# Optimization experiments

Hardware: AMD Instinct MI355X
Metric: run time of the kernel (lower is better)

The kernel has to match this reference:

```python
import jax, jax.numpy as jnp
import numpy as np


def setup_inputs() -> dict:
    key = jax.random.key(0)
    k1, k2, k3, k4 = jax.random.split(key, 4)
    B, N, F, T, K, O = 16, 1024, 16, 12, 3, 16
    x = jax.random.normal(k1, (B, N, F, T), dtype=jnp.float32)
    spatial_attention = jax.random.uniform(k2, (B, N, N), dtype=jnp.float32)
    adj = jax.random.uniform(k3, (N, N), dtype=jnp.float32)
    # xavier_uniform_ on [K, F, O]: bound = sqrt(6/(F+O)) over last two dims
    bound = float(np.sqrt(6.0 / (F + O)))
    Theta = jax.random.uniform(k4, (K, F, O), dtype=jnp.float32, minval=-bound, maxval=bound)
    return {"x": x, "spatial_attention": spatial_attention, "adj": adj, "Theta": Theta}


def reference(x, spatial_attention, adj, Theta):
    # x: [B, N, F, T], spatial_attention: [B, N, N], adj: [N, N], Theta: [K, F, O]
    B, N, F, T = x.shape
    K = Theta.shape[0]
    a = adj[None, :, :] * spatial_attention                      # [B, N, N]
    eye = jnp.broadcast_to(jnp.eye(N, dtype=x.dtype), (B, N, N))
    supports = [eye, a]
    for _ in range(2, K):                                        # power series of adjacency
        supports.append(jnp.matmul(supports[-1], a))
    S = jnp.stack(supports, axis=0)                              # [K, B, N, N]
    # rhs[k,b,n,f,t] = sum_m S[k,b,m,n] * x[b,m,f,t]  (supports[k]^T @ x), fused over T and K
    rhs = jnp.einsum('kbmn,bmft->kbnft', S, x)                   # [K, B, N, F, T]
    out = jnp.einsum('kbnft,kfo->bnot', rhs, Theta)              # [B, N, O, T]
    return jax.nn.relu(out)
```

## Files before the change

### kernel.cpp

```cpp
#include <hip/hip_runtime.h>
#include <hip/hip_bf16.h>


typedef __attribute__((ext_vector_type(8))) __bf16 bf16x8;
typedef __attribute__((ext_vector_type(4))) float  f32x4;
typedef __attribute__((ext_vector_type(8))) short  short8;
typedef __attribute__((ext_vector_type(4))) short  s16x4;

__device__ inline unsigned short f32_to_bf16(float f) {
    unsigned int u = __builtin_bit_cast(unsigned int, f);
    unsigned int r = u + 0x7FFFu + ((u >> 16) & 1u);
    return (unsigned short)(r >> 16);
}
__device__ inline float bf16_to_f32(unsigned short u) {
    unsigned int x = ((unsigned int)u) << 16;
    return __builtin_bit_cast(float, x);
}

__device__ inline void gload_lds16(const void* gsrc, void* ldst) {
    __builtin_amdgcn_global_load_lds(
        (const __attribute__((address_space(1))) unsigned int*)gsrc,
        (__attribute__((address_space(3))) unsigned int*)ldst,
        16, 0, 0);
}

__global__ void prep_a(const float* __restrict__ sa, const float* __restrict__ adj,
                       unsigned short* __restrict__ aT)
{
    __shared__ float tile[32][33];
    const int b  = blockIdx.z;
    const int m0 = blockIdx.y * 32;
    const int n0 = blockIdx.x * 32;
    const int tid = threadIdx.x;
    const int r  = tid >> 3;
    const int c4 = (tid & 7) * 4;
    const float* sab = sa + (size_t)b * 1024 * 1024;

    size_t idx = (size_t)(m0 + r) * 1024 + (n0 + c4);
    f32x4 av = *reinterpret_cast<const f32x4*>(&adj[idx]);
    f32x4 sv = *reinterpret_cast<const f32x4*>(&sab[idx]);
#pragma unroll
    for (int k = 0; k < 4; k++) tile[r][c4 + k] = av[k] * sv[k];
    __syncthreads();

    unsigned short* aTb = aT + (size_t)b * 1024 * 1024;
    const int nl = tid >> 3;
    const int m4 = (tid & 7) * 4;
    s16x4 v;
#pragma unroll
    for (int k = 0; k < 4; k++) v[k] = (short)f32_to_bf16(tile[m4 + k][nl]);
    *reinterpret_cast<s16x4*>(&aTb[(size_t)(n0 + nl) * 1024 + m0 + m4]) = v;
}

__global__ void prep_x(const float* __restrict__ x, unsigned short* __restrict__ xT)
{
    __shared__ float tile[32][33];
    const int b  = blockIdx.z;
    const int j0 = blockIdx.y * 32;
    const int m0 = blockIdx.x * 32;
    const int tid = threadIdx.x;
    const int r  = tid >> 3;
    const int c4 = (tid & 7) * 4;
    const float* xb = x + (size_t)b * 1024 * 192;

    f32x4 v = *reinterpret_cast<const f32x4*>(&xb[(size_t)(m0 + r) * 192 + j0 + c4]);
#pragma unroll
    for (int k = 0; k < 4; k++) tile[r][c4 + k] = v[k];
    __syncthreads();

    unsigned short* xTb = xT + (size_t)b * 192 * 1024;
    const int jl = tid >> 3;
    const int m4 = (tid & 7) * 4;
    s16x4 o;
#pragma unroll
    for (int k = 0; k < 4; k++) o[k] = (short)f32_to_bf16(tile[m4 + k][jl]);
    *reinterpret_cast<s16x4*>(&xTb[(size_t)(j0 + jl) * 1024 + m0 + m4]) = o;
}

__global__ __launch_bounds__(256, 2)
void gemm_tn(const unsigned short* __restrict__ Aop,
             const unsigned short* __restrict__ Bop,
             unsigned short* __restrict__ Cout)
{
    const int b  = blockIdx.z;
    const int j0 = blockIdx.y * 96;
    const int n0 = blockIdx.x * 64;
    const unsigned short* Ab = Aop + (size_t)b * 192 * 1024;
    const unsigned short* Bb = Bop + (size_t)b * 1024 * 1024;

    __shared__ unsigned short Blds[3][64 * 64];

    const int tid  = threadIdx.x;
    const int lane = tid & 63;
    const int wave = tid >> 6;
    const int wj   = wave >> 1;
    const int wn   = wave & 1;
    const int lr   = lane & 15;
    const int lg   = lane >> 4;

    const int srow = lane >> 3;
    const int sg16 = (lane & 7) ^ srow;

    f32x4 acc[3][2];
#pragma unroll
    for (int i = 0; i < 3; i++)
#pragma unroll
        for (int j = 0; j < 2; j++) acc[i][j] = f32x4{0.f, 0.f, 0.f, 0.f};

    const unsigned short* Arow[3];
#pragma unroll
    for (int ri = 0; ri < 3; ri++)
        Arow[ri] = Ab + (size_t)(j0 + wj * 48 + ri * 16 + lr) * 1024 + lg * 8;

    bf16x8 Ac[2][3], An[2][3];

#pragma unroll
    for (int i = 0; i < 2; i++) {
        int c = wave + i * 4;
        gload_lds16(Bb + (size_t)(n0 + 8 * c + srow) * 1024 + 0 + sg16 * 8,
                    &Blds[0][c * 512]);
    }
#pragma unroll
    for (int i = 0; i < 2; i++) {
        int c = wave + i * 4;
        gload_lds16(Bb + (size_t)(n0 + 8 * c + srow) * 1024 + 64 + sg16 * 8,
                    &Blds[1][c * 512]);
    }
#pragma unroll
    for (int h = 0; h < 2; h++)
#pragma unroll
        for (int ri = 0; ri < 3; ri++)
            Ac[h][ri] = __builtin_bit_cast(bf16x8,
                *reinterpret_cast<const short8*>(Arow[ri] + h * 32));
    __builtin_amdgcn_sched_barrier(0);
    asm volatile("s_waitcnt vmcnt(8)" ::: "memory");
    __builtin_amdgcn_s_barrier();
    __builtin_amdgcn_sched_barrier(0);

#pragma unroll
    for (int t = 0; t < 16; ++t) {
        const unsigned short* ldsB = &Blds[t % 3][0];
        bf16x8 Bfr[2][2];
#pragma unroll
        for (int h = 0; h < 2; h++)
#pragma unroll
            for (int ci = 0; ci < 2; ci++) {
                int row = wn * 32 + ci * 16 + lr;
                int sw  = (h * 4 + lg) ^ (lr & 7);
                Bfr[h][ci] = __builtin_bit_cast(bf16x8,
                    *reinterpret_cast<const short8*>(ldsB + row * 64 + sw * 8));
            }
        if (t < 14) {
#pragma unroll
            for (int i = 0; i < 2; i++) {
                int c = wave + i * 4;
                gload_lds16(Bb + (size_t)(n0 + 8 * c + srow) * 1024 + (t + 2) * 64 + sg16 * 8,
                            &Blds[(t + 2) % 3][c * 512]);
            }
        }
        if (t < 15) {
#pragma unroll
            for (int h = 0; h < 2; h++)
#pragma unroll
                for (int ri = 0; ri < 3; ri++)
                    An[h][ri] = __builtin_bit_cast(bf16x8,
                        *reinterpret_cast<const short8*>(Arow[ri] + (t + 1) * 64 + h * 32));
        }
#pragma unroll
        for (int h = 0; h < 2; h++)
#pragma unroll
            for (int ri = 0; ri < 3; ri++)
#pragma unroll
                for (int ci = 0; ci < 2; ci++)
                    acc[ri][ci] = __builtin_amdgcn_mfma_f32_16x16x32_bf16(
                        Ac[h][ri], Bfr[h][ci], acc[ri][ci], 0, 0, 0);
#pragma unroll
        for (int h = 0; h < 2; h++)
#pragma unroll
            for (int ri = 0; ri < 3; ri++)
                Ac[h][ri] = An[h][ri];
        asm volatile("s_waitcnt vmcnt(8)" ::: "memory");
        __builtin_amdgcn_s_barrier();
        __builtin_amdgcn_sched_barrier(0);
    }

    unsigned short* Cb = Cout + (size_t)b * 192 * 1024;
    const int jw = j0 + wj * 48;
    const int nw = n0 + wn * 32;
#pragma unroll
    for (int ri = 0; ri < 3; ri++)
#pragma unroll
        for (int ci = 0; ci < 2; ci++) {
            int col = nw + ci * 16 + lr;
#pragma unroll
            for (int r = 0; r < 4; r++) {
                int row = jw + ri * 16 + lg * 4 + r;
                Cb[(size_t)row * 1024 + col] = f32_to_bf16(acc[ri][ci][r]);
            }
        }
}

#define OBUF_STRIDE 196

__global__ __launch_bounds__(192)
void final_contract(const unsigned short* __restrict__ xT,
                    const unsigned short* __restrict__ r1,
                    const unsigned short* __restrict__ r2,
                    const float* __restrict__ Theta,
                    float* __restrict__ out)
{
    __shared__ float th[768];
    __shared__ float obuf[64 * OBUF_STRIDE];

    const int tid = threadIdx.x;
    for (int i = tid; i < 768; i += 192) th[i] = Theta[i];
    __syncthreads();

    const int b  = blockIdx.y;
    const int n0 = blockIdx.x * 64;
    const int nl = tid & 63;
    const int tq = tid >> 6;

    float acc[4][16];
#pragma unroll
    for (int tt = 0; tt < 4; tt++)
#pragma unroll
        for (int o = 0; o < 16; o++) acc[tt][o] = 0.f;

    const size_t basep = (size_t)b * 192 * 1024 + n0 + nl;
#pragma unroll
    for (int f = 0; f < 16; f++) {
        size_t off = basep + (size_t)(f * 12 + tq * 4) * 1024;
        float v0[4], v1[4], v2[4];
#pragma unroll
        for (int tt = 0; tt < 4; tt++) {
            v0[tt] = bf16_to_f32(xT[off + (size_t)tt * 1024]);
            v1[tt] = bf16_to_f32(r1[off + (size_t)tt * 1024]);
            v2[tt] = bf16_to_f32(r2[off + (size_t)tt * 1024]);
        }
        const f32x4* t0 = reinterpret_cast<const f32x4*>(&th[0 * 256 + f * 16]);
        const f32x4* t1 = reinterpret_cast<const f32x4*>(&th[1 * 256 + f * 16]);
        const f32x4* t2 = reinterpret_cast<const f32x4*>(&th[2 * 256 + f * 16]);
#pragma unroll
        for (int q = 0; q < 4; q++) {
            f32x4 w0 = t0[q], w1 = t1[q], w2 = t2[q];
#pragma unroll
            for (int tt = 0; tt < 4; tt++)
#pragma unroll
                for (int e = 0; e < 4; e++)
                    acc[tt][q * 4 + e] += v0[tt] * w0[e] + v1[tt] * w1[e] + v2[tt] * w2[e];
        }
    }
#pragma unroll
    for (int o = 0; o < 16; o++) {
        f32x4 v;
#pragma unroll
        for (int tt = 0; tt < 4; tt++) v[tt] = fmaxf(acc[tt][o], 0.f);
        *reinterpret_cast<f32x4*>(&obuf[nl * OBUF_STRIDE + o * 12 + tq * 4]) = v;
    }
    __syncthreads();

    float* outp = out + ((size_t)b * 1024 + n0) * 192;
#pragma unroll
    for (int i = 0; i < 16; i++) {
        int v   = tid + i * 192;
        int row = v / 48;
        int c   = v - row * 48;
        *reinterpret_cast<f32x4*>(&outp[(size_t)v * 4]) =
            *reinterpret_cast<const f32x4*>(&obuf[row * OBUF_STRIDE + c * 4]);
    }
}

extern "C" void kernel_launch(void* const* d_in, const int* in_sizes, int n_in,
                              void* d_out, int out_size, void* d_ws, size_t ws_size,
                              hipStream_t stream)
{
    const float* x     = (const float*)d_in[0];
    const float* sa    = (const float*)d_in[1];
    const float* adj   = (const float*)d_in[2];
    const float* Theta = (const float*)d_in[3];
    float* out = (float*)d_out;

    char* ws = (char*)d_ws;
    const size_t SZ_AT = (size_t)16 * 1024 * 1024 * 2;
    const size_t SZ_XT = (size_t)16 * 192  * 1024 * 2;
    unsigned short* aT = (unsigned short*)ws;
    unsigned short* xT = (unsigned short*)(ws + SZ_AT);
    unsigned short* r1 = (unsigned short*)(ws + SZ_AT + SZ_XT);
    unsigned short* r2 = (unsigned short*)(ws + SZ_AT + 2 * SZ_XT);

    prep_a<<<dim3(32, 32, 16), 256, 0, stream>>>(sa, adj, aT);
    prep_x<<<dim3(32, 6, 16), 256, 0, stream>>>(x, xT);
    gemm_tn<<<dim3(16, 2, 16), 256, 0, stream>>>(xT, aT, r1);
    gemm_tn<<<dim3(16, 2, 16), 256, 0, stream>>>(r1, aT, r2);
    final_contract<<<dim3(16, 16), 192, 0, stream>>>(xT, r1, r2, Theta, out);
}
```

Baseline: 95.14 us.

## Widen GEMM tile to 128 columns, swizzle block order, stage output through LDS

The batched TN GEMM now gives each block 96x128 output instead of 96x64, so every block reads more of the B operand per A fragment and the grid is halved to 256 blocks. Block indices are swizzled so that neighbouring blocks in launch order fall on different batches, and the epilogue writes bf16 results into LDS and then stores them to global memory as coalesced 16-byte rows. It also reorders the A prefetch ahead of the B async loads and adjusts the vmcnt waits. The costs are more accumulator registers, occupancy limited to one block per SIMD set, and only 256 blocks on 256 CUs, which weakens latency hiding.

```diff
diff --git a/kernel.cpp b/kernel.cpp
--- a/kernel.cpp
+++ b/kernel.cpp
@@ -77,18 +77,23 @@
     *reinterpret_cast<s16x4*>(&xTb[(size_t)(j0 + jl) * 1024 + m0 + m4]) = o;
 }
 
-__global__ __launch_bounds__(256, 2)
+__global__ __launch_bounds__(256, 1)
 void gemm_tn(const unsigned short* __restrict__ Aop,
              const unsigned short* __restrict__ Bop,
              unsigned short* __restrict__ Cout)
 {
-    const int b  = blockIdx.z;
-    const int j0 = blockIdx.y * 96;
-    const int n0 = blockIdx.x * 64;
+    const int lin = blockIdx.x + 8 * (blockIdx.y + 2 * blockIdx.z);
+    const int swz = (lin & 7) * 32 + (lin >> 3);
+    const int nb  = swz & 7;
+    const int jb  = (swz >> 3) & 1;
+    const int b   = swz >> 4;
+
+    const int j0 = jb * 96;
+    const int n0 = nb * 128;
     const unsigned short* Ab = Aop + (size_t)b * 192 * 1024;
     const unsigned short* Bb = Bop + (size_t)b * 1024 * 1024;
 
-    __shared__ unsigned short Blds[3][64 * 64];
+    __shared__ unsigned short Blds[3][128 * 64];
 
     const int tid  = threadIdx.x;
     const int lane = tid & 63;
@@ -101,11 +106,11 @@
     const int srow = lane >> 3;
     const int sg16 = (lane & 7) ^ srow;
 
-    f32x4 acc[3][2];
+    f32x4 acc[3][4];
 #pragma unroll
     for (int i = 0; i < 3; i++)
 #pragma unroll
-        for (int j = 0; j < 2; j++) acc[i][j] = f32x4{0.f, 0.f, 0.f, 0.f};
+        for (int j = 0; j < 4; j++) acc[i][j] = f32x4{0.f, 0.f, 0.f, 0.f};
 
     const unsigned short* Arow[3];
 #pragma unroll
@@ -115,14 +120,14 @@
     bf16x8 Ac[2][3], An[2][3];
 
 #pragma unroll
-    for (int i = 0; i < 2; i++) {
-        int c = wave + i * 4;
+    for (int i = 0; i < 4; i++) {
+        int c = wave * 4 + i;
         gload_lds16(Bb + (size_t)(n0 + 8 * c + srow) * 1024 + 0 + sg16 * 8,
                     &Blds[0][c * 512]);
     }
 #pragma unroll
-    for (int i = 0; i < 2; i++) {
-        int c = wave + i * 4;
+    for (int i = 0; i < 4; i++) {
+        int c = wave * 4 + i;
         gload_lds16(Bb + (size_t)(n0 + 8 * c + srow) * 1024 + 64 + sg16 * 8,
                     &Blds[1][c * 512]);
     }
@@ -133,45 +138,48 @@
             Ac[h][ri] = __builtin_bit_cast(bf16x8,
                 *reinterpret_cast<const short8*>(Arow[ri] + h * 32));
     __builtin_amdgcn_sched_barrier(0);
-    asm volatile("s_waitcnt vmcnt(8)" ::: "memory");
+    asm volatile("s_waitcnt vmcnt(10)" ::: "memory");
     __builtin_amdgcn_s_barrier();
     __builtin_amdgcn_sched_barrier(0);
 
 #pragma unroll
     for (int t = 0; t < 16; ++t) {
         const unsigned short* ldsB = &Blds[t % 3][0];
-        bf16x8 Bfr[2][2];
+        bf16x8 Bfr[2][4];
 #pragma unroll
         for (int h = 0; h < 2; h++)
 #pragma unroll
-            for (int ci = 0; ci < 2; ci++) {
-                int row = wn * 32 + ci * 16 + lr;
+            for (int ci = 0; ci < 4; ci++) {
+                int row = wn * 64 + ci * 16 + lr;
                 int sw  = (h * 4 + lg) ^ (lr & 7);
                 Bfr[h][ci] = __builtin_bit_cast(bf16x8,
                     *reinterpret_cast<const short8*>(ldsB + row * 64 + sw * 8));
             }
+        __builtin_amdgcn_sched_barrier(0);
+        if (t < 15) {
+#pragma unroll
+            for (int h = 0; h < 2; h++)
+#pragma unroll
+                for (int ri = 0; ri < 3; ri++)
+                    An[h][ri] = __builtin_bit_cast(bf16x8,
+                        *reinterpret_cast<const short8*>(Arow[ri] + (t + 1) * 64 + h * 32));
+        }
+        __builtin_amdgcn_sched_barrier(0);
         if (t < 14) {
 #pragma unroll
-            for (int i = 0; i < 2; i++) {
-                int c = wave + i * 4;
+            for (int i = 0; i < 4; i++) {
+                int c = wave * 4 + i;
                 gload_lds16(Bb + (size_t)(n0 + 8 * c + srow) * 1024 + (t + 2) * 64 + sg16 * 8,
                             &Blds[(t + 2) % 3][c * 512]);
             }
         }
-        if (t < 15) {
-#pragma unroll
-            for (int h = 0; h < 2; h++)
-#pragma unroll
-                for (int ri = 0; ri < 3; ri++)
-                    An[h][ri] = __builtin_bit_cast(bf16x8,
-                        *reinterpret_cast<const short8*>(Arow[ri] + (t + 1) * 64 + h * 32));
-        }
+        __builtin_amdgcn_sched_barrier(0);
 #pragma unroll
         for (int h = 0; h < 2; h++)
 #pragma unroll
             for (int ri = 0; ri < 3; ri++)
 #pragma unroll
-                for (int ci = 0; ci < 2; ci++)
+                for (int ci = 0; ci < 4; ci++)
                     acc[ri][ci] = __builtin_amdgcn_mfma_f32_16x16x32_bf16(
                         Ac[h][ri], Bfr[h][ci], acc[ri][ci], 0, 0, 0);
 #pragma unroll
@@ -179,25 +187,40 @@
 #pragma unroll
             for (int ri = 0; ri < 3; ri++)
                 Ac[h][ri] = An[h][ri];
-        asm volatile("s_waitcnt vmcnt(8)" ::: "memory");
-        __builtin_amdgcn_s_barrier();
-        __builtin_amdgcn_sched_barrier(0);
-    }
-
+        if (t < 14) {
+            asm volatile("s_waitcnt vmcnt(10)" ::: "memory");
+            __builtin_amdgcn_s_barrier();
+            __builtin_amdgcn_sched_barrier(0);
+        } else if (t == 14) {
+            asm volatile("s_waitcnt vmcnt(6)" ::: "memory");
+            __builtin_amdgcn_s_barrier();
+            __builtin_amdgcn_sched_barrier(0);
+        }
+    }
+
+    __syncthreads();
+    unsigned short* cl = (unsigned short*)&Blds[0][0];
+#pragma unroll
+    for (int ri = 0; ri < 3; ri++)
+#pragma unroll
+        for (int ci = 0; ci < 4; ci++) {
+            int col = wn * 64 + ci * 16 + lr;
+#pragma unroll
+            for (int r = 0; r < 4; r++) {
+                int row = wj * 48 + ri * 16 + lg * 4 + r;
+                cl[row * 128 + col] = f32_to_bf16(acc[ri][ci][r]);
+            }
+        }
+    __syncthreads();
     unsigned short* Cb = Cout + (size_t)b * 192 * 1024;
-    const int jw = j0 + wj * 48;
-    const int nw = n0 + wn * 32;
-#pragma unroll
-    for (int ri = 0; ri < 3; ri++)
-#pragma unroll
-        for (int ci = 0; ci < 2; ci++) {
-            int col = nw + ci * 16 + lr;
-#pragma unroll
-            for (int r = 0; r < 4; r++) {
-                int row = jw + ri * 16 + lg * 4 + r;
-                Cb[(size_t)row * 1024 + col] = f32_to_bf16(acc[ri][ci][r]);
-            }
-        }
+#pragma unroll
+    for (int i = 0; i < 6; i++) {
+        int idx = tid + i * 256;
+        int row = idx >> 4;
+        int c16 = idx & 15;
+        *reinterpret_cast<short8*>(Cb + (size_t)(j0 + row) * 1024 + n0 + c16 * 8) =
+            *reinterpret_cast<const short8*>(cl + row * 128 + c16 * 8);
+    }
 }
 
 #define OBUF_STRIDE 196
@@ -291,7 +314,7 @@
 
     prep_a<<<dim3(32, 32, 16), 256, 0, stream>>>(sa, adj, aT);
     prep_x<<<dim3(32, 6, 16), 256, 0, stream>>>(x, xT);
-    gemm_tn<<<dim3(16, 2, 16), 256, 0, stream>>>(xT, aT, r1);
-    gemm_tn<<<dim3(16, 2, 16), 256, 0, stream>>>(r1, aT, r2);
+    gemm_tn<<<dim3(8, 2, 16), 256, 0, stream>>>(xT, aT, r1);
+    gemm_tn<<<dim3(8, 2, 16), 256, 0, stream>>>(r1, aT, r2);
     final_contract<<<dim3(16, 16), 192, 0, stream>>>(xT, r1, r2, Theta, out);
 }
```

Result: faster. 82.99 us (-12.8%).
